# Kernel optimization log

Hardware: AMD Instinct MI355X
Metric: run time of the kernel (lower is better)

The kernel has to match this reference:

```python
import jax, jax.numpy as jnp
import numpy as np

B, S, H, NH, DIS = 8, 512, 512, 8, 32
HD = H // NH  # head_dim = 64


def setup_inputs() -> dict:
    key = jax.random.key(0)
    ks = jax.random.split(key, 9)
    sc = 0.05
    return {
        "x": jax.random.normal(ks[0], (B, S, H), jnp.float32),
        "rel_distance": jax.random.randint(ks[1], (B, S, 2 * S), 0, DIS, jnp.int64),
        "mask": jnp.zeros((B, S, 2 * S), jnp.bool_),
        "query_pos_embedding": jax.random.normal(ks[2], (DIS, H), jnp.float32) * sc,
        "key_pos_embedding": jax.random.normal(ks[3], (DIS, H), jnp.float32) * sc,
        "value_pos_embedding": jax.random.normal(ks[4], (DIS, H), jnp.float32) * sc,
        "Wq": jax.random.normal(ks[5], (H, H), jnp.float32) * sc,
        "Wk": jax.random.normal(ks[6], (2 * H, H), jnp.float32) * sc,
        "Wv": jax.random.normal(ks[7], (2 * H, H), jnp.float32) * sc,
        "Wo": jax.random.normal(ks[8], (H, H), jnp.float32) * sc,
    }


def reference(x, rel_distance, mask, query_pos_embedding, key_pos_embedding,
              value_pos_embedding, Wq, Wk, Wv, Wo):
    b, s, _ = x.shape
    scale = jnp.sqrt(jnp.asarray(HD, x.dtype))

    # projections (torch Linear: y = x @ W.T)
    q = (x @ Wq.T).reshape(b, s, NH, HD).transpose(0, 2, 1, 3)        # [B,h,S,d]
    k = (x @ Wk.T).reshape(b, 2 * s, NH, HD).transpose(0, 2, 1, 3)    # [B,h,2S,d]
    v = (x @ Wv.T).reshape(b, 2 * s, NH, HD).transpose(0, 2, 1, 3)    # [B,h,2S,d]

    rel = jnp.broadcast_to(rel_distance[:, None], (b, NH, s, 2 * s))  # [B,h,S,2S]

    # relative-position weights via gather along distance axis
    q_emb = query_pos_embedding.reshape(DIS, NH, HD)                  # [n,h,d]
    qpw_full = jnp.einsum('bhsd,nhd->bhsn', q, q_emb)                 # [B,h,S,n]
    qpw = jnp.take_along_axis(qpw_full, rel, axis=3)                  # [B,h,S,2S]

    k_emb = key_pos_embedding.reshape(DIS, NH, HD)
    kpw_full = jnp.einsum('bhkd,nhd->bhkn', k, k_emb)                 # [B,h,2S,n]
    kpw = jnp.take_along_axis(kpw_full, rel.transpose(0, 1, 3, 2), axis=3)  # [B,h,2S,S]
    kpw = kpw.transpose(0, 1, 3, 2)                                   # [B,h,S,2S]

    scores = (jnp.einsum('bhsd,bhkd->bhsk', q, k) + qpw + kpw) / scale
    scores = jnp.where(mask[:, None], -jnp.inf, scores)
    probs = jax.nn.softmax(scores, axis=-1)                           # [B,h,S,2S]

    # scatter-add probs into distance buckets: [B,h,S,n]
    bi = jnp.arange(b)[:, None, None, None]
    hi = jnp.arange(NH)[None, :, None, None]
    si = jnp.arange(s)[None, None, :, None]
    vdw = jnp.zeros((b, NH, s, DIS), probs.dtype).at[bi, hi, si, rel].add(probs)

    v_emb = value_pos_embedding.reshape(DIS, NH, HD)                  # [n,h,d]
    out = jnp.einsum('bhsk,bhkd->bhsd', probs, v) \
        + jnp.einsum('bhsn,nhd->bhsd', vdw, v_emb)                    # [B,h,S,d]
    out = out.transpose(0, 2, 1, 3).reshape(b, s, H)
    return out @ Wo.T
```

## Files before the change

### kernel.cpp

```cpp
#include <hip/hip_runtime.h>
#include <math.h>

#define Bc 8
#define Sc 512
#define Hc 512
#define NHc 8
#define HDc 64
#define DISc 32
#define S2c 1024

typedef __attribute__((ext_vector_type(8))) short bf16x8;
typedef __attribute__((ext_vector_type(4))) float f32x4;
#define MFMA16(a, b, c) __builtin_amdgcn_mfma_f32_16x16x32_bf16(a, b, c, 0, 0, 0)

__device__ __forceinline__ unsigned short f2bf(float f) {
  unsigned u = __float_as_uint(f);
  return (unsigned short)((u + 0x7fffu + ((u >> 16) & 1u)) >> 16);
}
__device__ __forceinline__ float b2f(unsigned short u) {
  return __uint_as_float((unsigned)u << 16);
}
__device__ __forceinline__ bf16x8 ldb16x8(const unsigned short* p) {
  union { uint4 u; bf16x8 s; } cv;
  cv.u = *(const uint4*)p;
  return cv.s;
}

__global__ __launch_bounds__(256) void cvt5_k(
    const float* __restrict__ x, const float* __restrict__ wq,
    const float* __restrict__ wk, const float* __restrict__ wv,
    const float* __restrict__ wo, unsigned short* __restrict__ x16,
    unsigned short* __restrict__ w16q, unsigned short* __restrict__ w16k,
    unsigned short* __restrict__ w16v, unsigned short* __restrict__ w16o) {
  int i = blockIdx.x * 256 + threadIdx.x;
  const float* src; unsigned short* dst; int off;
  if (i < 524288)      { src = x;  dst = x16;  off = i; }
  else if (i < 589824) { src = wq; dst = w16q; off = i - 524288; }
  else if (i < 720896) { src = wk; dst = w16k; off = i - 589824; }
  else if (i < 851968) { src = wv; dst = w16v; off = i - 720896; }
  else                 { src = wo; dst = w16o; off = i - 851968; }
  float4 v = ((const float4*)src)[off];
  ushort4 u;
  u.x = f2bf(v.x); u.y = f2bf(v.y); u.z = f2bf(v.z); u.w = f2bf(v.w);
  ((ushort4*)dst)[off] = u;
}

__global__ __launch_bounds__(256) void pack_k(const int* __restrict__ rel,
                                              const unsigned char* __restrict__ mask,
                                              unsigned char* __restrict__ pk8) {
  int i = blockIdx.x * 256 + threadIdx.x;
  const int* rp = rel + i * 16;
  uint4 mu = *(const uint4*)(mask + i * 16);
  const unsigned char* mb = (const unsigned char*)&mu;
  uint4 o;
  unsigned* ow = (unsigned*)&o;
#pragma unroll
  for (int g = 0; g < 4; ++g) {
    int4 r4 = ((const int4*)rp)[g];
    unsigned b0 = ((unsigned)r4.x & 31u) | (mb[g * 4 + 0] ? 0x80u : 0u);
    unsigned b1 = ((unsigned)r4.y & 31u) | (mb[g * 4 + 1] ? 0x80u : 0u);
    unsigned b2 = ((unsigned)r4.z & 31u) | (mb[g * 4 + 2] ? 0x80u : 0u);
    unsigned b3 = ((unsigned)r4.w & 31u) | (mb[g * 4 + 3] ? 0x80u : 0u);
    ow[g] = b0 | (b1 << 8) | (b2 << 16) | (b3 << 24);
  }
  *(uint4*)(pk8 + i * 16) = o;
}

template <int MODE>
__global__ __launch_bounds__(256, 4) void gemm16_k(
    const unsigned short* __restrict__ A, const unsigned short* __restrict__ B,
    void* __restrict__ outp, int M, int N, int K) {
  const int t = threadIdx.x;
  const int w = t >> 6, lane = t & 63, ln = lane & 15, qd = lane >> 4;
  const int wm = (w >> 1) << 5, wn = (w & 1) << 5;
  const int m0 = blockIdx.y << 6, n0 = blockIdx.x << 6;
  __shared__ unsigned short As[64 * 32];
  __shared__ unsigned short Bs[64 * 32];
  f32x4 z = {0.f, 0.f, 0.f, 0.f};
  f32x4 acc[2][2] = {{z, z}, {z, z}};
  const int srow = t >> 2, sc8 = (t & 3) << 3;
  for (int k0 = 0; k0 < K; k0 += 32) {
    *(uint4*)&As[srow * 32 + sc8] = *(const uint4*)(A + (size_t)(m0 + srow) * K + k0 + sc8);
    *(uint4*)&Bs[srow * 32 + sc8] = *(const uint4*)(B + (size_t)(n0 + srow) * K + k0 + sc8);
    __syncthreads();
    bf16x8 a0 = ldb16x8(&As[(wm + ln) * 32 + qd * 8]);
    bf16x8 a1 = ldb16x8(&As[(wm + 16 + ln) * 32 + qd * 8]);
    bf16x8 b0 = ldb16x8(&Bs[(wn + ln) * 32 + qd * 8]);
    bf16x8 b1 = ldb16x8(&Bs[(wn + 16 + ln) * 32 + qd * 8]);
    acc[0][0] = MFMA16(a0, b0, acc[0][0]);
    acc[0][1] = MFMA16(a0, b1, acc[0][1]);
    acc[1][0] = MFMA16(a1, b0, acc[1][0]);
    acc[1][1] = MFMA16(a1, b1, acc[1][1]);
    __syncthreads();
  }
#pragma unroll
  for (int tm = 0; tm < 2; ++tm)
#pragma unroll
    for (int tn = 0; tn < 2; ++tn)
#pragma unroll
      for (int r = 0; r < 4; ++r) {
        int m = m0 + wm + tm * 16 + qd * 4 + r;
        int n = n0 + wn + tn * 16 + ln;
        float v = acc[tm][tn][r];
        if (MODE == 0) {
          ((float*)outp)[(size_t)m * N + n] = v;
        } else {
          int bb = m >> 9, s = m & 511, hh = (n >> 6) & 7, d = n & 63;
          if (MODE == 1)
            ((unsigned short*)outp)[((size_t)(bb * 8 + hh) * 512 + s) * 64 + d] = f2bf(v);
          else if (MODE == 2) {
            int k2 = 2 * s + (n >> 9);
            ((unsigned short*)outp)[((size_t)(bb * 8 + hh) * 1024 + k2) * 64 + d] = f2bf(v);
          } else {
            int k2 = 2 * s + (n >> 9);
            ((unsigned short*)outp)[((size_t)(bb * 8 + hh) * 64 + d) * 1024 + k2] = f2bf(v);
          }
        }
      }
}

__global__ __launch_bounds__(256) void posw16_k(const unsigned short* __restrict__ rows16,
                                                const float* __restrict__ emb,
                                                float* __restrict__ out, int R) {
  const int t = threadIdx.x;
  const int tiles = R >> 6;
  const int rt = blockIdx.x % tiles;
  const int h = (blockIdx.x / tiles) & 7;
  const int b = blockIdx.x / (tiles * 8);
  __shared__ float es[32][65];
  __shared__ float xs[64][65];
#pragma unroll
  for (int i = 0; i < 2; ++i) {
    int f = t + (i << 8);
    int n = f >> 4, d4 = (f & 15) << 2;
    float4 v4 = *(const float4*)(emb + ((size_t)n << 9) + (h << 6) + d4);
    es[n][d4] = v4.x; es[n][d4 + 1] = v4.y; es[n][d4 + 2] = v4.z; es[n][d4 + 3] = v4.w;
  }
  const size_t row0 = (size_t)(b * 8 + h) * R + (rt << 6);
#pragma unroll
  for (int p = 0; p < 2; ++p) {
    int id = t + (p << 8);
    int r = id >> 3, c8 = (id & 7) << 3;
    uint4 u4 = *(const uint4*)(rows16 + (row0 + r) * 64 + c8);
    const unsigned short* us = (const unsigned short*)&u4;
#pragma unroll
    for (int j = 0; j < 8; ++j) xs[r][c8 + j] = b2f(us[j]);
  }
  __syncthreads();
  const int n = t & 31;
  const int rs0 = (t >> 5) << 3;
  for (int rr = 0; rr < 8; ++rr) {
    float s = 0.f;
#pragma unroll
    for (int d = 0; d < 64; ++d) s = fmaf(xs[rs0 + rr][d], es[n][d], s);
    out[((((size_t)b * 8 + h) * R) + (rt << 6) + rs0 + rr) * 32 + n] = s;
  }
}

__global__ __launch_bounds__(512, 4) void attn5_k(
    const unsigned short* __restrict__ q16h, const unsigned short* __restrict__ kb16,
    const unsigned short* __restrict__ vT16, const float* __restrict__ qpw,
    const float* __restrict__ kpw, const unsigned char* __restrict__ pk8,
    const float* __restrict__ v_emb, unsigned short* __restrict__ attn16) {
  const int bid = blockIdx.x;
  const int b = bid & 7;
  const int h = (bid >> 3) & 7;
  const int qb = ((bid >> 6) & 7) << 6;
  const int t = threadIdx.x;
  const int w = t >> 6;
  const int g = w >> 2;
  const int ws4 = w & 3;
  const int lane = t & 63;
  const int ln = lane & 15;
  const int qd = lane >> 4;

  __shared__ __align__(16) char smem[60928];
  unsigned char*  pkt  = (unsigned char*)smem;
  unsigned short* kpws = (unsigned short*)(smem + 10240);
  unsigned short* q32s = (unsigned short*)(smem + 19456);
  unsigned short* pbuf = (unsigned short*)(smem + 24064);
  unsigned long long* vdwm64 = (unsigned long long*)(smem + 42496);
  float*          accbuf = (float*)smem;
  unsigned short* vest   = (unsigned short*)(smem + 24064);
  unsigned short* vdwb   = (unsigned short*)(smem + 29184);

  for (int i = t; i < 4 * 16 * 36; i += 512) vdwm64[i] = 0ull;
  {
    const float* src = qpw + ((size_t)((b * 8 + h) * 512 + qb)) * 32;
    int row = t >> 3, c4 = (t & 7) << 2;
    float4 v = *(const float4*)(src + row * 32 + c4);
    ushort4 u;
    u.x = f2bf(v.x); u.y = f2bf(v.y); u.z = f2bf(v.z); u.w = f2bf(v.w);
    *(ushort4*)&q32s[row * 36 + c4] = u;
  }
  const unsigned short* kbase = kb16 + (size_t)(b * 8 + h) * 65536;
  const unsigned short* vbase = vT16 + (size_t)(b * 8 + h) * 65536;
  bf16x8 aQ[2];
  {
    const unsigned short* qsrc =
        q16h + ((size_t)((b * 8 + h) * 512 + qb + ws4 * 16 + ln)) * 64;
    aQ[0] = ldb16x8(qsrc + qd * 8);
    aQ[1] = ldb16x8(qsrc + 32 + qd * 8);
  }
  f32x4 z = {0.f, 0.f, 0.f, 0.f};
  f32x4 acc[4] = {z, z, z, z};

  for (int kti = 0; kti < 8; ++kti) {
    {
      int u = t & 255, gg = t >> 8;
      int kt0s = (kti + gg * 8) << 6;
      unsigned char* pt_ = pkt + gg * 5120;
      unsigned short* kp_ = kpws + gg * 2304;
      int qr = u >> 2, cg = (u & 3) << 4;
      uint4 pv = *(const uint4*)(pk8 + ((size_t)(b * 512 + qb + qr)) * 1024 + kt0s + cg);
      *(uint4*)&pt_[qr * 80 + cg] = pv;
      int krow = u >> 2, kc8 = (u & 3) << 3;
      const float* kpp = kpw + ((size_t)((b * 8 + h) * 1024) + kt0s + krow) * 32 + kc8;
      float4 f0 = *(const float4*)kpp;
      float4 f1 = *(const float4*)(kpp + 4);
      ushort4 u0, u1;
      u0.x = f2bf(f0.x); u0.y = f2bf(f0.y); u0.z = f2bf(f0.z); u0.w = f2bf(f0.w);
      u1.x = f2bf(f1.x); u1.y = f2bf(f1.y); u1.z = f2bf(f1.z); u1.w = f2bf(f1.w);
      *(ushort4*)&kp_[krow * 36 + kc8] = u0;
      *(ushort4*)&kp_[krow * 36 + kc8 + 4] = u1;
    }
    __syncthreads();
    const int kt0 = (kti + g * 8) << 6;

    f32x4 sc4[4];
#pragma unroll
    for (int t4 = 0; t4 < 4; ++t4) {
      f32x4 c = z;
      c = MFMA16(aQ[0], ldb16x8(kbase + (size_t)(kt0 + t4 * 16 + ln) * 64 + qd * 8), c);
      c = MFMA16(aQ[1], ldb16x8(kbase + (size_t)(kt0 + t4 * 16 + ln) * 64 + 32 + qd * 8), c);
      sc4[t4] = c;
    }

    unsigned char* pt_ = pkt + g * 5120;
    unsigned short* kp_ = kpws + g * 2304;
#pragma unroll
    for (int r = 0; r < 4; ++r) {
#pragma unroll
      for (int t4 = 0; t4 < 4; ++t4) {
        int row_l = ws4 * 16 + qd * 4 + r;
        int kl = t4 * 16 + ln;
        unsigned um = pt_[row_l * 80 + kl];
        int rd = um & 31;
        float s = (sc4[t4][r] + b2f(q32s[row_l * 36 + rd]) + b2f(kp_[kl * 36 + rd])) * 0.125f;
        float p = (um & 0x80u) ? 0.f : __expf(s);
        atomicAdd(&vdwm64[ws4 * 576 + (qd * 4 + r) * 36 + rd],
                  (unsigned long long)(p * 67108864.0f));
        pbuf[w * 1152 + (qd * 4 + r) * 72 + kl] = f2bf(p);
      }
    }

    bf16x8 a0 = ldb16x8(&pbuf[w * 1152 + ln * 72 + qd * 8]);
    bf16x8 a1 = ldb16x8(&pbuf[w * 1152 + ln * 72 + 32 + qd * 8]);
#pragma unroll
    for (int dt = 0; dt < 4; ++dt) {
      acc[dt] = MFMA16(a0, ldb16x8(vbase + (size_t)(dt * 16 + ln) * 1024 + kt0 + qd * 8), acc[dt]);
      acc[dt] = MFMA16(a1, ldb16x8(vbase + (size_t)(dt * 16 + ln) * 1024 + kt0 + 32 + qd * 8), acc[dt]);
    }
    __syncthreads();
  }

  if (t < 256) {
    int n = t >> 3, d0 = (t & 7) << 3;
    const float* src = v_emb + ((size_t)n << 9) + (h << 6) + d0;
    float4 f0 = *(const float4*)src;
    float4 f1 = *(const float4*)(src + 4);
    vest[(d0 + 0) * 40 + n] = f2bf(f0.x); vest[(d0 + 1) * 40 + n] = f2bf(f0.y);
    vest[(d0 + 2) * 40 + n] = f2bf(f0.z); vest[(d0 + 3) * 40 + n] = f2bf(f0.w);
    vest[(d0 + 4) * 40 + n] = f2bf(f1.x); vest[(d0 + 5) * 40 + n] = f2bf(f1.y);
    vest[(d0 + 6) * 40 + n] = f2bf(f1.z); vest[(d0 + 7) * 40 + n] = f2bf(f1.w);
  } else {
    int row = lane >> 2, n0 = (lane & 3) << 3;
    float vv[8];
#pragma unroll
    for (int j = 0; j < 8; ++j)
      vv[j] = (float)vdwm64[ws4 * 576 + row * 36 + n0 + j] * 1.4901161193847656e-8f;
    ushort4 u0, u1;
    u0.x = f2bf(vv[0]); u0.y = f2bf(vv[1]); u0.z = f2bf(vv[2]); u0.w = f2bf(vv[3]);
    u1.x = f2bf(vv[4]); u1.y = f2bf(vv[5]); u1.z = f2bf(vv[6]); u1.w = f2bf(vv[7]);
    *(ushort4*)&vdwb[ws4 * 640 + row * 40 + n0] = u0;
    *(ushort4*)&vdwb[ws4 * 640 + row * 40 + n0 + 4] = u1;
  }
  __syncthreads();

  if (g == 1) {
    bf16x8 av = ldb16x8(&vdwb[ws4 * 640 + ln * 40 + qd * 8]);
#pragma unroll
    for (int dt = 0; dt < 4; ++dt)
      acc[dt] = MFMA16(av, ldb16x8(&vest[(dt * 16 + ln) * 40 + qd * 8]), acc[dt]);
#pragma unroll
    for (int r = 0; r < 4; ++r)
#pragma unroll
      for (int dt = 0; dt < 4; ++dt)
        accbuf[ws4 * 1088 + (qd * 4 + r) * 68 + dt * 16 + ln] = acc[dt][r];
  }
  __syncthreads();

  if (g == 0) {
    float inv[4];
#pragma unroll
    for (int r = 0; r < 4; ++r) {
      unsigned long long lu = 0ull;
#pragma unroll
      for (int n = 0; n < 32; ++n)
        lu += vdwm64[ws4 * 576 + (qd * 4 + r) * 36 + n];
      inv[r] = 67108864.0f / (float)lu;
    }
    unsigned short* obase =
        attn16 + ((size_t)(b * 512 + qb + ws4 * 16 + qd * 4)) * 512 + (h << 6);
#pragma unroll
    for (int r = 0; r < 4; ++r)
#pragma unroll
      for (int dt = 0; dt < 4; ++dt) {
        float v = (acc[dt][r] + accbuf[ws4 * 1088 + (qd * 4 + r) * 68 + dt * 16 + ln]) * inv[r];
        obase[(size_t)r * 512 + dt * 16 + ln] = f2bf(v);
      }
  }
}

extern "C" void kernel_launch(void* const* d_in, const int* in_sizes, int n_in,
                              void* d_out, int out_size, void* d_ws, size_t ws_size,
                              hipStream_t stream) {
  const float* x = (const float*)d_in[0];
  const int* rel = (const int*)d_in[1];
  const unsigned char* mask = (const unsigned char*)d_in[2];
  const float* qpe = (const float*)d_in[3];
  const float* kpe = (const float*)d_in[4];
  const float* vpe = (const float*)d_in[5];
  const float* Wq = (const float*)d_in[6];
  const float* Wk = (const float*)d_in[7];
  const float* Wv = (const float*)d_in[8];
  const float* Wo = (const float*)d_in[9];
  float* out = (float*)d_out;

  float* ws = (float*)d_ws;
  float* qpw = ws;
  float* kpw = qpw + 1048576;
  unsigned short* kb16 = (unsigned short*)(kpw + 2097152);
  unsigned short* vT16 = kb16 + 4194304;
  unsigned short* q16h = vT16 + 4194304;
  unsigned short* attn16 = q16h + 2097152;
  unsigned short* x16 = attn16 + 2097152;
  unsigned short* w16q = x16 + 2097152;
  unsigned short* w16k = w16q + 262144;
  unsigned short* w16v = w16k + 524288;
  unsigned short* w16o = w16v + 524288;
  unsigned char* pk8 = (unsigned char*)(w16o + 262144);

  pack_k<<<1024, 256, 0, stream>>>(rel, mask, pk8);
  cvt5_k<<<3584, 256, 0, stream>>>(x, Wq, Wk, Wv, Wo, x16, w16q, w16k, w16v, w16o);
  gemm16_k<1><<<dim3(8, 64), 256, 0, stream>>>(x16, w16q, q16h, 4096, 512, 512);
  gemm16_k<2><<<dim3(16, 64), 256, 0, stream>>>(x16, w16k, kb16, 4096, 1024, 512);
  gemm16_k<3><<<dim3(16, 64), 256, 0, stream>>>(x16, w16v, vT16, 4096, 1024, 512);
  posw16_k<<<8 * 8 * 8, 256, 0, stream>>>(q16h, qpe, qpw, 512);
  posw16_k<<<8 * 8 * 16, 256, 0, stream>>>(kb16, kpe, kpw, 1024);
  attn5_k<<<512, 512, 0, stream>>>(q16h, kb16, vT16, qpw, kpw, pk8, vpe, attn16);
  gemm16_k<0><<<dim3(8, 64), 256, 0, stream>>>(attn16, w16o, out, 4096, 512, 512);
}
```

Baseline: 238.1 us.

## Fold positional-embedding projections into QK GEMMs and prefetch tiles in GEMM/attention

Precomputes emb·W products so the query/key positional weights come out of the Q and K projection GEMMs as extra output columns in bf16, which removes the two separate posw kernels and their fp32 intermediates. Folds the 1/sqrt(d) scale into Wq and the Q-side embedding weights. The GEMM now uses a K-tile of 64 with register prefetch of the next tile and padded shared-memory rows, and the attention kernel prefetches the next mask/kpw tile into registers. The cost is extra GEMM columns and some bf16 rounding of the combined weights.

```diff
diff --git a/kernel.cpp b/kernel.cpp
--- a/kernel.cpp
+++ b/kernel.cpp
@@ -33,15 +33,16 @@
     unsigned short* __restrict__ w16q, unsigned short* __restrict__ w16k,
     unsigned short* __restrict__ w16v, unsigned short* __restrict__ w16o) {
   int i = blockIdx.x * 256 + threadIdx.x;
-  const float* src; unsigned short* dst; int off;
+  const float* src; unsigned short* dst; int off; float sc = 1.f;
   if (i < 524288)      { src = x;  dst = x16;  off = i; }
-  else if (i < 589824) { src = wq; dst = w16q; off = i - 524288; }
+  else if (i < 589824) { src = wq; dst = w16q; off = i - 524288; sc = 0.125f; }
   else if (i < 720896) { src = wk; dst = w16k; off = i - 589824; }
   else if (i < 851968) { src = wv; dst = w16v; off = i - 720896; }
   else                 { src = wo; dst = w16o; off = i - 851968; }
   float4 v = ((const float4*)src)[off];
   ushort4 u;
-  u.x = f2bf(v.x); u.y = f2bf(v.y); u.z = f2bf(v.z); u.w = f2bf(v.w);
+  u.x = f2bf(v.x * sc); u.y = f2bf(v.y * sc);
+  u.z = f2bf(v.z * sc); u.w = f2bf(v.w * sc);
   ((ushort4*)dst)[off] = u;
 }
 
@@ -66,31 +67,106 @@
   *(uint4*)(pk8 + i * 16) = o;
 }
 
+__global__ __launch_bounds__(256) void wemb_k(
+    const float* __restrict__ qpe, const float* __restrict__ kpe,
+    const float* __restrict__ Wq, const float* __restrict__ Wk,
+    unsigned short* __restrict__ wqp, unsigned short* __restrict__ wkp) {
+  const int bid = blockIdx.x;
+  const int cc = bid & 3, unit = bid >> 2;
+  const int c0 = cc << 7;
+  const int t = threadIdx.x;
+  const float* emb; const float* Wsrc; unsigned short* outp; int rowbase, h;
+  if (unit < 8) {
+    h = unit; emb = qpe; Wsrc = Wq + (size_t)(h * 64) * 512; outp = wqp; rowbase = h * 32;
+  } else {
+    int u = unit - 8; int e = u >> 3; h = u & 7;
+    emb = kpe; Wsrc = Wk + (size_t)(e * 512 + h * 64) * 512; outp = wkp;
+    rowbase = e * 256 + h * 32;
+  }
+  __shared__ float es[32][65];
+  __shared__ float wsh[64][132];
+  {
+    int n = t >> 3, d4 = (t & 7) << 3;
+    float4 v0 = *(const float4*)(emb + (size_t)n * 512 + h * 64 + d4);
+    float4 v1 = *(const float4*)(emb + (size_t)n * 512 + h * 64 + d4 + 4);
+    *(float4*)&es[n][d4] = v0;
+    *(float4*)&es[n][d4 + 4] = v1;
+  }
+#pragma unroll
+  for (int p = 0; p < 8; ++p) {
+    int slot = t + (p << 8);
+    int d = slot >> 5, c4 = (slot & 31) << 2;
+    *(float4*)&wsh[d][c4] = *(const float4*)(Wsrc + (size_t)d * 512 + c0 + c4);
+  }
+  __syncthreads();
+  const int n = t >> 3, cb = (t & 7) << 4;
+  float acc[16] = {};
+#pragma unroll
+  for (int d = 0; d < 64; ++d) {
+    float ev = es[n][d];
+    float4 w0 = *(const float4*)&wsh[d][cb];
+    float4 w1 = *(const float4*)&wsh[d][cb + 4];
+    float4 w2 = *(const float4*)&wsh[d][cb + 8];
+    float4 w3 = *(const float4*)&wsh[d][cb + 12];
+    acc[0] = fmaf(ev, w0.x, acc[0]);   acc[1] = fmaf(ev, w0.y, acc[1]);
+    acc[2] = fmaf(ev, w0.z, acc[2]);   acc[3] = fmaf(ev, w0.w, acc[3]);
+    acc[4] = fmaf(ev, w1.x, acc[4]);   acc[5] = fmaf(ev, w1.y, acc[5]);
+    acc[6] = fmaf(ev, w1.z, acc[6]);   acc[7] = fmaf(ev, w1.w, acc[7]);
+    acc[8] = fmaf(ev, w2.x, acc[8]);   acc[9] = fmaf(ev, w2.y, acc[9]);
+    acc[10] = fmaf(ev, w2.z, acc[10]); acc[11] = fmaf(ev, w2.w, acc[11]);
+    acc[12] = fmaf(ev, w3.x, acc[12]); acc[13] = fmaf(ev, w3.y, acc[13]);
+    acc[14] = fmaf(ev, w3.z, acc[14]); acc[15] = fmaf(ev, w3.w, acc[15]);
+  }
+  unsigned short* orow = outp + (size_t)(rowbase + n) * 512 + c0 + cb;
+#pragma unroll
+  for (int j = 0; j < 16; ++j) orow[j] = f2bf(acc[j] * 0.125f);
+}
+
 template <int MODE>
 __global__ __launch_bounds__(256, 4) void gemm16_k(
-    const unsigned short* __restrict__ A, const unsigned short* __restrict__ B,
-    void* __restrict__ outp, int M, int N, int K) {
+    const unsigned short* __restrict__ A, const unsigned short* __restrict__ B1,
+    const unsigned short* __restrict__ B2, void* __restrict__ out1,
+    void* __restrict__ out2, int M, int N, int K, int nsplit) {
   const int t = threadIdx.x;
   const int w = t >> 6, lane = t & 63, ln = lane & 15, qd = lane >> 4;
   const int wm = (w >> 1) << 5, wn = (w & 1) << 5;
   const int m0 = blockIdx.y << 6, n0 = blockIdx.x << 6;
-  __shared__ unsigned short As[64 * 32];
-  __shared__ unsigned short Bs[64 * 32];
+  __shared__ unsigned short As[64 * 72];
+  __shared__ unsigned short Bs[64 * 72];
+  const bool reg1 = (n0 < nsplit);
+  const unsigned short* Bb =
+      reg1 ? B1 + (size_t)n0 * K : B2 + (size_t)(n0 - nsplit) * K;
+  const int r0 = t >> 3, c8 = (t & 7) << 3;
+  const unsigned short* ga = A + (size_t)(m0 + r0) * K + c8;
+  const unsigned short* gb = Bb + (size_t)r0 * K + c8;
+  const size_t half = (size_t)32 * K;
+  uint4 va0 = *(const uint4*)ga, va1 = *(const uint4*)(ga + half);
+  uint4 vb0 = *(const uint4*)gb, vb1 = *(const uint4*)(gb + half);
   f32x4 z = {0.f, 0.f, 0.f, 0.f};
   f32x4 acc[2][2] = {{z, z}, {z, z}};
-  const int srow = t >> 2, sc8 = (t & 3) << 3;
-  for (int k0 = 0; k0 < K; k0 += 32) {
-    *(uint4*)&As[srow * 32 + sc8] = *(const uint4*)(A + (size_t)(m0 + srow) * K + k0 + sc8);
-    *(uint4*)&Bs[srow * 32 + sc8] = *(const uint4*)(B + (size_t)(n0 + srow) * K + k0 + sc8);
+  for (int k0 = 0; k0 < K; k0 += 64) {
+    *(uint4*)&As[r0 * 72 + c8] = va0;
+    *(uint4*)&As[(r0 + 32) * 72 + c8] = va1;
+    *(uint4*)&Bs[r0 * 72 + c8] = vb0;
+    *(uint4*)&Bs[(r0 + 32) * 72 + c8] = vb1;
     __syncthreads();
-    bf16x8 a0 = ldb16x8(&As[(wm + ln) * 32 + qd * 8]);
-    bf16x8 a1 = ldb16x8(&As[(wm + 16 + ln) * 32 + qd * 8]);
-    bf16x8 b0 = ldb16x8(&Bs[(wn + ln) * 32 + qd * 8]);
-    bf16x8 b1 = ldb16x8(&Bs[(wn + 16 + ln) * 32 + qd * 8]);
-    acc[0][0] = MFMA16(a0, b0, acc[0][0]);
-    acc[0][1] = MFMA16(a0, b1, acc[0][1]);
-    acc[1][0] = MFMA16(a1, b0, acc[1][0]);
-    acc[1][1] = MFMA16(a1, b1, acc[1][1]);
+    if (k0 + 64 < K) {
+      va0 = *(const uint4*)(ga + k0 + 64);
+      va1 = *(const uint4*)(ga + half + k0 + 64);
+      vb0 = *(const uint4*)(gb + k0 + 64);
+      vb1 = *(const uint4*)(gb + half + k0 + 64);
+    }
+#pragma unroll
+    for (int kk = 0; kk < 64; kk += 32) {
+      bf16x8 a0 = ldb16x8(&As[(wm + ln) * 72 + kk + qd * 8]);
+      bf16x8 a1 = ldb16x8(&As[(wm + 16 + ln) * 72 + kk + qd * 8]);
+      bf16x8 b0 = ldb16x8(&Bs[(wn + ln) * 72 + kk + qd * 8]);
+      bf16x8 b1 = ldb16x8(&Bs[(wn + 16 + ln) * 72 + kk + qd * 8]);
+      acc[0][0] = MFMA16(a0, b0, acc[0][0]);
+      acc[0][1] = MFMA16(a0, b1, acc[0][1]);
+      acc[1][0] = MFMA16(a1, b0, acc[1][0]);
+      acc[1][1] = MFMA16(a1, b1, acc[1][1]);
+    }
     __syncthreads();
   }
 #pragma unroll
@@ -102,65 +178,39 @@
         int m = m0 + wm + tm * 16 + qd * 4 + r;
         int n = n0 + wn + tn * 16 + ln;
         float v = acc[tm][tn][r];
+        int bb = m >> 9, s = m & 511;
         if (MODE == 0) {
-          ((float*)outp)[(size_t)m * N + n] = v;
+          ((float*)out1)[(size_t)m * N + n] = v;
+        } else if (MODE == 3) {
+          int e = n >> 9, hh = (n >> 6) & 7, d = n & 63;
+          int k2 = 2 * s + e;
+          ((unsigned short*)out1)[((size_t)(bb * 8 + hh) * 64 + d) * 1024 + k2] = f2bf(v);
+        } else if (MODE == 1) {
+          if (reg1) {
+            int hh = (n >> 6) & 7, d = n & 63;
+            ((unsigned short*)out1)[((size_t)(bb * 8 + hh) * 512 + s) * 64 + d] = f2bf(v);
+          } else {
+            int n2 = n - 512, hh = n2 >> 5, nn = n2 & 31;
+            ((unsigned short*)out2)[((size_t)(bb * 8 + hh) * 512 + s) * 32 + nn] = f2bf(v);
+          }
         } else {
-          int bb = m >> 9, s = m & 511, hh = (n >> 6) & 7, d = n & 63;
-          if (MODE == 1)
-            ((unsigned short*)outp)[((size_t)(bb * 8 + hh) * 512 + s) * 64 + d] = f2bf(v);
-          else if (MODE == 2) {
-            int k2 = 2 * s + (n >> 9);
-            ((unsigned short*)outp)[((size_t)(bb * 8 + hh) * 1024 + k2) * 64 + d] = f2bf(v);
+          if (reg1) {
+            int e = n >> 9, hh = (n >> 6) & 7, d = n & 63;
+            int k2 = 2 * s + e;
+            ((unsigned short*)out1)[((size_t)(bb * 8 + hh) * 1024 + k2) * 64 + d] = f2bf(v);
           } else {
-            int k2 = 2 * s + (n >> 9);
-            ((unsigned short*)outp)[((size_t)(bb * 8 + hh) * 64 + d) * 1024 + k2] = f2bf(v);
+            int n2 = n - 1024, e = n2 >> 8, hh = (n2 >> 5) & 7, nn = n2 & 31;
+            int k2 = 2 * s + e;
+            ((unsigned short*)out2)[((size_t)(bb * 8 + hh) * 1024 + k2) * 32 + nn] = f2bf(v);
           }
         }
       }
 }
 
-__global__ __launch_bounds__(256) void posw16_k(const unsigned short* __restrict__ rows16,
-                                                const float* __restrict__ emb,
-                                                float* __restrict__ out, int R) {
-  const int t = threadIdx.x;
-  const int tiles = R >> 6;
-  const int rt = blockIdx.x % tiles;
-  const int h = (blockIdx.x / tiles) & 7;
-  const int b = blockIdx.x / (tiles * 8);
-  __shared__ float es[32][65];
-  __shared__ float xs[64][65];
-#pragma unroll
-  for (int i = 0; i < 2; ++i) {
-    int f = t + (i << 8);
-    int n = f >> 4, d4 = (f & 15) << 2;
-    float4 v4 = *(const float4*)(emb + ((size_t)n << 9) + (h << 6) + d4);
-    es[n][d4] = v4.x; es[n][d4 + 1] = v4.y; es[n][d4 + 2] = v4.z; es[n][d4 + 3] = v4.w;
-  }
-  const size_t row0 = (size_t)(b * 8 + h) * R + (rt << 6);
-#pragma unroll
-  for (int p = 0; p < 2; ++p) {
-    int id = t + (p << 8);
-    int r = id >> 3, c8 = (id & 7) << 3;
-    uint4 u4 = *(const uint4*)(rows16 + (row0 + r) * 64 + c8);
-    const unsigned short* us = (const unsigned short*)&u4;
-#pragma unroll
-    for (int j = 0; j < 8; ++j) xs[r][c8 + j] = b2f(us[j]);
-  }
-  __syncthreads();
-  const int n = t & 31;
-  const int rs0 = (t >> 5) << 3;
-  for (int rr = 0; rr < 8; ++rr) {
-    float s = 0.f;
-#pragma unroll
-    for (int d = 0; d < 64; ++d) s = fmaf(xs[rs0 + rr][d], es[n][d], s);
-    out[((((size_t)b * 8 + h) * R) + (rt << 6) + rs0 + rr) * 32 + n] = s;
-  }
-}
-
-__global__ __launch_bounds__(512, 4) void attn5_k(
+__global__ __launch_bounds__(512, 4) void attn6_k(
     const unsigned short* __restrict__ q16h, const unsigned short* __restrict__ kb16,
-    const unsigned short* __restrict__ vT16, const float* __restrict__ qpw,
-    const float* __restrict__ kpw, const unsigned char* __restrict__ pk8,
+    const unsigned short* __restrict__ vT16, const unsigned short* __restrict__ qpw16,
+    const unsigned short* __restrict__ kpw16, const unsigned char* __restrict__ pk8,
     const float* __restrict__ v_emb, unsigned short* __restrict__ attn16) {
   const int bid = blockIdx.x;
   const int b = bid & 7;
@@ -185,13 +235,10 @@
   unsigned short* vdwb   = (unsigned short*)(smem + 29184);
 
   for (int i = t; i < 4 * 16 * 36; i += 512) vdwm64[i] = 0ull;
-  {
-    const float* src = qpw + ((size_t)((b * 8 + h) * 512 + qb)) * 32;
-    int row = t >> 3, c4 = (t & 7) << 2;
-    float4 v = *(const float4*)(src + row * 32 + c4);
-    ushort4 u;
-    u.x = f2bf(v.x); u.y = f2bf(v.y); u.z = f2bf(v.z); u.w = f2bf(v.w);
-    *(ushort4*)&q32s[row * 36 + c4] = u;
+  if (t < 256) {
+    int row = t >> 2, c8 = (t & 3) << 3;
+    *(uint4*)&q32s[row * 36 + c8] =
+        *(const uint4*)(qpw16 + ((size_t)((b * 8 + h) * 512 + qb) + row) * 32 + c8);
   }
   const unsigned short* kbase = kb16 + (size_t)(b * 8 + h) * 65536;
   const unsigned short* vbase = vT16 + (size_t)(b * 8 + h) * 65536;
@@ -205,26 +252,26 @@
   f32x4 z = {0.f, 0.f, 0.f, 0.f};
   f32x4 acc[4] = {z, z, z, z};
 
+  const int u = t & 255, gg = t >> 8;
+  const int qr = u >> 2, cg = (u & 3) << 4;
+  const int kc8 = (u & 3) << 3;
+  const unsigned char* pks = pk8 + ((size_t)(b * 512 + qb + qr)) * 1024 + (gg << 9);
+  const unsigned short* kps =
+      kpw16 + ((size_t)((b * 8 + h) * 1024) + (gg << 9) + qr) * 32 + kc8;
+  unsigned char* pt_w = pkt + gg * 5120 + qr * 80 + cg;
+  unsigned short* kp_w = kpws + gg * 2304 + qr * 36 + kc8;
+
+  uint4 pv = *(const uint4*)(pks + cg);
+  uint4 kv = *(const uint4*)kps;
+
   for (int kti = 0; kti < 8; ++kti) {
-    {
-      int u = t & 255, gg = t >> 8;
-      int kt0s = (kti + gg * 8) << 6;
-      unsigned char* pt_ = pkt + gg * 5120;
-      unsigned short* kp_ = kpws + gg * 2304;
-      int qr = u >> 2, cg = (u & 3) << 4;
-      uint4 pv = *(const uint4*)(pk8 + ((size_t)(b * 512 + qb + qr)) * 1024 + kt0s + cg);
-      *(uint4*)&pt_[qr * 80 + cg] = pv;
-      int krow = u >> 2, kc8 = (u & 3) << 3;
-      const float* kpp = kpw + ((size_t)((b * 8 + h) * 1024) + kt0s + krow) * 32 + kc8;
-      float4 f0 = *(const float4*)kpp;
-      float4 f1 = *(const float4*)(kpp + 4);
-      ushort4 u0, u1;
-      u0.x = f2bf(f0.x); u0.y = f2bf(f0.y); u0.z = f2bf(f0.z); u0.w = f2bf(f0.w);
-      u1.x = f2bf(f1.x); u1.y = f2bf(f1.y); u1.z = f2bf(f1.z); u1.w = f2bf(f1.w);
-      *(ushort4*)&kp_[krow * 36 + kc8] = u0;
-      *(ushort4*)&kp_[krow * 36 + kc8 + 4] = u1;
-    }
+    *(uint4*)pt_w = pv;
+    *(uint4*)kp_w = kv;
     __syncthreads();
+    if (kti < 7) {
+      pv = *(const uint4*)(pks + ((kti + 1) << 6) + cg);
+      kv = *(const uint4*)(kps + ((size_t)(kti + 1) << 11));
+    }
     const int kt0 = (kti + g * 8) << 6;
 
     f32x4 sc4[4];
@@ -246,7 +293,7 @@
         int kl = t4 * 16 + ln;
         unsigned um = pt_[row_l * 80 + kl];
         int rd = um & 31;
-        float s = (sc4[t4][r] + b2f(q32s[row_l * 36 + rd]) + b2f(kp_[kl * 36 + rd])) * 0.125f;
+        float s = sc4[t4][r] + b2f(q32s[row_l * 36 + rd]) + b2f(kp_[kl * 36 + rd]);
         float p = (um & 0x80u) ? 0.f : __expf(s);
         atomicAdd(&vdwm64[ws4 * 576 + (qd * 4 + r) * 36 + rd],
                   (unsigned long long)(p * 67108864.0f));
@@ -337,27 +384,32 @@
   const float* Wo = (const float*)d_in[9];
   float* out = (float*)d_out;
 
-  float* ws = (float*)d_ws;
-  float* qpw = ws;
-  float* kpw = qpw + 1048576;
-  unsigned short* kb16 = (unsigned short*)(kpw + 2097152);
-  unsigned short* vT16 = kb16 + 4194304;
-  unsigned short* q16h = vT16 + 4194304;
-  unsigned short* attn16 = q16h + 2097152;
-  unsigned short* x16 = attn16 + 2097152;
-  unsigned short* w16q = x16 + 2097152;
-  unsigned short* w16k = w16q + 262144;
-  unsigned short* w16v = w16k + 524288;
-  unsigned short* w16o = w16v + 524288;
-  unsigned char* pk8 = (unsigned char*)(w16o + 262144);
+  unsigned short* u = (unsigned short*)d_ws;
+  unsigned short* x16    = u;
+  unsigned short* w16q   = x16 + 2097152;
+  unsigned short* w16k   = w16q + 262144;
+  unsigned short* w16v   = w16k + 524288;
+  unsigned short* w16o   = w16v + 524288;
+  unsigned short* wqp16  = w16o + 262144;
+  unsigned short* wkp16  = wqp16 + 131072;
+  unsigned short* q16h   = wkp16 + 262144;
+  unsigned short* qpw16  = q16h + 2097152;
+  unsigned short* kb16   = qpw16 + 1048576;
+  unsigned short* kpw16  = kb16 + 4194304;
+  unsigned short* vT16   = kpw16 + 2097152;
+  unsigned short* attn16 = vT16 + 4194304;
+  unsigned char* pk8 = (unsigned char*)(attn16 + 2097152);
 
   pack_k<<<1024, 256, 0, stream>>>(rel, mask, pk8);
   cvt5_k<<<3584, 256, 0, stream>>>(x, Wq, Wk, Wv, Wo, x16, w16q, w16k, w16v, w16o);
-  gemm16_k<1><<<dim3(8, 64), 256, 0, stream>>>(x16, w16q, q16h, 4096, 512, 512);
-  gemm16_k<2><<<dim3(16, 64), 256, 0, stream>>>(x16, w16k, kb16, 4096, 1024, 512);
-  gemm16_k<3><<<dim3(16, 64), 256, 0, stream>>>(x16, w16v, vT16, 4096, 1024, 512);
-  posw16_k<<<8 * 8 * 8, 256, 0, stream>>>(q16h, qpe, qpw, 512);
-  posw16_k<<<8 * 8 * 16, 256, 0, stream>>>(kb16, kpe, kpw, 1024);
-  attn5_k<<<512, 512, 0, stream>>>(q16h, kb16, vT16, qpw, kpw, pk8, vpe, attn16);
-  gemm16_k<0><<<dim3(8, 64), 256, 0, stream>>>(attn16, w16o, out, 4096, 512, 512);
-}
+  wemb_k<<<96, 256, 0, stream>>>(qpe, kpe, Wq, Wk, wqp16, wkp16);
+  gemm16_k<1><<<dim3(12, 64), 256, 0, stream>>>(x16, w16q, wqp16, q16h, qpw16,
+                                                4096, 768, 512, 512);
+  gemm16_k<2><<<dim3(24, 64), 256, 0, stream>>>(x16, w16k, wkp16, kb16, kpw16,
+                                                4096, 1536, 512, 1024);
+  gemm16_k<3><<<dim3(16, 64), 256, 0, stream>>>(x16, w16v, nullptr, vT16, nullptr,
+                                                4096, 1024, 512, 1024);
+  attn6_k<<<512, 512, 0, stream>>>(q16h, kb16, vT16, qpw16, kpw16, pk8, vpe, attn16);
+  gemm16_k<0><<<dim3(8, 64), 256, 0, stream>>>(attn16, w16o, nullptr, out, nullptr,
+                                               4096, 512, 512, 512);
+}
```

After: 220.8 us. -7.3%, faster.
